# Optimization experiments

Measured on AMD Instinct MI355X. Metric: run time of the kernel, lower is better.

The kernel has to match this reference:

```python
import jax, jax.numpy as jnp
import numpy as np

I_DIM, L_DIM, H_DIM, O_DIM = 1024, 1024, 2048, 512
HALT_H = max(4, H_DIM // 2)
BATCH = 4096


def setup_inputs() -> dict:
    key = jax.random.key(0)
    ks = jax.random.split(key, 14)
    s = 0.02
    gin = I_DIM + O_DIM
    jdim = L_DIM + O_DIM
    return {
        "inputs": jax.random.normal(ks[0], (BATCH, I_DIM), jnp.float32),
        "W_ih": jax.random.normal(ks[1], (3 * L_DIM, gin), jnp.float32) * s,
        "W_hh": jax.random.normal(ks[2], (3 * L_DIM, L_DIM), jnp.float32) * s,
        "b_ih": jax.random.normal(ks[3], (3 * L_DIM,), jnp.float32) * s,
        "b_hh": jax.random.normal(ks[4], (3 * L_DIM,), jnp.float32) * s,
        "aw1": jax.random.normal(ks[5], (H_DIM, jdim), jnp.float32) * s,
        "ab1": jax.random.normal(ks[6], (H_DIM,), jnp.float32) * s,
        "aw2": jax.random.normal(ks[7], (O_DIM, H_DIM), jnp.float32) * s,
        "ab2": jax.random.normal(ks[8], (O_DIM,), jnp.float32) * s,
        "hw1": jax.random.normal(ks[9], (HALT_H, jdim), jnp.float32) * s,
        "hb1": jax.random.normal(ks[10], (HALT_H,), jnp.float32) * s,
        "hw2": jax.random.normal(ks[11], (2, HALT_H), jnp.float32) * s,
        "hb2": jax.random.normal(ks[12], (2,), jnp.float32) * s,
        "inner_cycles": 4,
        "outer_steps": 8,
    }


def reference(inputs, W_ih, W_hh, b_ih, b_hh, aw1, ab1, aw2, ab2,
              hw1, hb1, hw2, hb2, inner_cycles, outer_steps):
    B = inputs.shape[0]
    L = W_hh.shape[1]
    O = aw2.shape[0]

    def gru_step(state, x_gates):
        # PyTorch GRUCell: gates ordered (r, z, n)
        h_gates = state @ W_hh.T + b_hh  # [B, 3L]
        xr, xz, xn = jnp.split(x_gates, 3, axis=-1)
        hr, hz, hn = jnp.split(h_gates, 3, axis=-1)
        r = jax.nn.sigmoid(xr + hr)
        z = jax.nn.sigmoid(xz + hz)
        n = jnp.tanh(xn + r * hn)
        return (1.0 - z) * n + z * state

    def outer(carry, _):
        state, ans = carry
        # gru_input is constant over inner cycles -> hoist input projection
        x = jnp.concatenate([inputs, ans], axis=-1)       # [B, I+O]
        x_gates = x @ W_ih.T + b_ih                        # [B, 3L]

        def inner(s, _):
            return gru_step(s, x_gates), None

        state, _ = jax.lax.scan(inner, state, None, length=inner_cycles)
        joint = jnp.concatenate([state, ans], axis=-1)     # [B, L+O]
        h1 = jax.nn.relu(joint @ aw1.T + ab1)
        logits = h1 @ aw2.T + ab2                          # [B, O]
        ans_new = jnp.tanh(logits)
        h2 = jax.nn.relu(joint @ hw1.T + hb1)
        halt = h2 @ hw2.T + hb2                            # [B, 2]
        return (state, ans_new), (logits, halt)

    state0 = jnp.zeros((B, L), inputs.dtype)
    ans0 = jnp.zeros((B, O), inputs.dtype)
    _, (answer_logits, halt_logits) = jax.lax.scan(
        outer, (state0, ans0), None, length=outer_steps)
    # stacked equivalents of the per-step lists: [outer_steps, B, O], [outer_steps, B, 2]
    return answer_logits, halt_logits
```

## Files before the change

kernel.cpp:

```cpp
#include <hip/hip_runtime.h>
#include <math.h>

#define BATCH 4096
#define LDIM 1024
#define HDIM 2048
#define ODIM 512
#define GDIM 3072
#define JDIM 1536
#define INNER 4
#define OUTER 8

using f16 = _Float16;
using f16x4 = __attribute__((ext_vector_type(4))) _Float16;
using f16x8 = __attribute__((ext_vector_type(8))) _Float16;
using f32x4 = __attribute__((ext_vector_type(4))) float;

typedef __attribute__((address_space(3))) void lds_void;
typedef __attribute__((address_space(1))) void glob_void;

__device__ __forceinline__ void gload16(const void* g, void* l) {
  __builtin_amdgcn_global_load_lds((const glob_void*)g, (lds_void*)l, 16, 0, 0);
}

#define MFMA16(a, b, c) __builtin_amdgcn_mfma_f32_16x16x32_f16(a, b, c, 0, 0, 0)
#define WAIT_VM(N) asm volatile("s_waitcnt vmcnt(" #N ")" ::: "memory")
#define SBAR asm volatile("s_barrier" ::: "memory")

__device__ __forceinline__ float fast_sigmoid(float x) {
  return __builtin_amdgcn_rcpf(1.0f + __expf(-x));
}
__device__ __forceinline__ float fast_tanh(float x) {
  return 1.0f - 2.0f * __builtin_amdgcn_rcpf(1.0f + __expf(2.0f * x));
}

__global__ __launch_bounds__(256) void convert_w(const float* __restrict__ src,
                                                 f16* __restrict__ dst, int n4) {
  int i = blockIdx.x * 256 + threadIdx.x;
  if (i >= n4) return;
  float4 v = ((const float4*)src)[i];
  f16x4 d = {(f16)v.x, (f16)v.y, (f16)v.z, (f16)v.w};
  *(f16x4*)&dst[(size_t)i * 4] = d;
}

__global__ __launch_bounds__(256) void input_to_cat(
    const float* __restrict__ inp, f16* __restrict__ cH) {
  int idx = blockIdx.x * 256 + threadIdx.x;
  if (idx >= BATCH * 256) return;
  int row = idx >> 8, c4 = idx & 255;
  float4 v = ((const float4*)inp)[idx];
  f16x4 h4 = {(f16)v.x, (f16)v.y, (f16)v.z, (f16)v.w};
  *(f16x4*)&cH[(size_t)row * JDIM + c4 * 4] = h4;
}

template <int EPI>
__global__ __launch_bounds__(512, 1) void gemm_f16(
    const f16* __restrict__ A, const f16* __restrict__ W,
    const float* __restrict__ bias, const float* __restrict__ bias2,
    f16* __restrict__ Ch, float* __restrict__ Cf, int N, int K) {
  __shared__ f16 sA[2 * 2 * 256 * 32];
  __shared__ f16 sW[2 * 2 * 256 * 32];
  const int tid = threadIdx.x;
  const int w = tid >> 6, lane = tid & 63;
  const int wm = w >> 2, wn = w & 3;
  const int fr = lane & 15, quad = lane >> 4;
  const int nb = N >> 8;
  const int m0 = (blockIdx.x / nb) * 256, n0 = (blockIdx.x % nb) * 256;

  const int swz_src = (((tid & 3) ^ ((tid >> 3) & 3)) * 8);
  const f16* pAst = A + (size_t)(m0 + (tid >> 2)) * K + swz_src;
  const f16* pWst = W + (size_t)(n0 + (tid >> 2)) * K + swz_src;
  const size_t h128 = (size_t)128 * K;
  const int ldst = tid * 8;
  const int swr = ((quad ^ ((fr >> 1) & 3)) * 8);

  f32x4 acc[8][4] = {};
  const int NT = K >> 6;

#define STA(p, kh, kt)                                              \
  {                                                                 \
    int o = ((p) * 2 + (kh)) * 8192 + ldst;                         \
    gload16(pAst + (kt) * 64 + (kh) * 32, &sA[o]);                  \
    gload16(pAst + h128 + (kt) * 64 + (kh) * 32, &sA[o + 4096]);    \
  }
#define STW(p, kh, kt)                                              \
  {                                                                 \
    int o = ((p) * 2 + (kh)) * 8192 + ldst;                         \
    gload16(pWst + (kt) * 64 + (kh) * 32, &sW[o]);                  \
    gload16(pWst + h128 + (kt) * 64 + (kh) * 32, &sW[o + 4096]);    \
  }
#define LDB(p, kk)                                                  \
  _Pragma("unroll") for (int j = 0; j < 4; ++j) {                   \
    int rn = wn * 64 + j * 16 + fr;                                 \
    bf[j] = *(const f16x8*)&sW[((p) * 2 + (kk)) * 8192 + rn * 32 + swr]; \
  }
#define LDA(p, kk, mh)                                              \
  _Pragma("unroll") for (int i2 = 0; i2 < 4; ++i2) {                \
    int rm = wm * 128 + (mh) * 64 + i2 * 16 + fr;                   \
    af[i2] = *(const f16x8*)&sA[((p) * 2 + (kk)) * 8192 + rm * 32 + swr]; \
  }
#define DOMFMA(mh)                                                  \
  __builtin_amdgcn_s_setprio(1);                                    \
  _Pragma("unroll") for (int i2 = 0; i2 < 4; ++i2)                  \
  _Pragma("unroll") for (int j = 0; j < 4; ++j)                     \
      acc[(mh) * 4 + i2][j] = MFMA16(af[i2], bf[j], acc[(mh) * 4 + i2][j]); \
  __builtin_amdgcn_s_setprio(0);

  STA(0, 0, 0); STW(0, 0, 0); STA(0, 1, 0); STW(0, 1, 0);

  for (int t = 0; t < NT; ++t) {
    const int p = t & 1, pn = p ^ 1;
    const bool pf = (t + 1 < NT);
    f16x8 af[4], bf[4];
    if (t == NT - 1) { WAIT_VM(0); } else { WAIT_VM(4); }
    SBAR;
    if (pf) STA(pn, 0, t + 1);
    LDB(p, 0); LDA(p, 0, 0);
    DOMFMA(0);
    SBAR;
    if (pf) STW(pn, 0, t + 1);
    LDA(p, 0, 1);
    DOMFMA(1);
    if (t == NT - 1) { WAIT_VM(0); } else { WAIT_VM(4); }
    SBAR;
    if (pf) STA(pn, 1, t + 1);
    LDB(p, 1); LDA(p, 1, 0);
    DOMFMA(0);
    SBAR;
    if (pf) STW(pn, 1, t + 1);
    LDA(p, 1, 1);
    DOMFMA(1);
  }
#undef STA
#undef STW
#undef LDB
#undef LDA
#undef DOMFMA

  bool is_h1 = true;
  const float* bp = bias;
  int nb0 = n0;
  if (EPI == 1) {
    is_h1 = (n0 < 2048);
    bp = is_h1 ? bias : bias2;
    nb0 = is_h1 ? n0 : n0 - 2048;
  }
#pragma unroll
  for (int j = 0; j < 4; ++j) {
    int n = nb0 + wn * 64 + j * 16 + fr;
    float bv = bp[n];
#pragma unroll
    for (int i = 0; i < 8; ++i) {
      int mb = m0 + wm * 128 + i * 16 + quad * 4;
      if (EPI == 0) {
        f16x4 o = {(f16)(acc[i][j][0] + bv), (f16)(acc[i][j][1] + bv),
                   (f16)(acc[i][j][2] + bv), (f16)(acc[i][j][3] + bv)};
        *(f16x4*)&Ch[((size_t)(mb >> 2) * N + n) * 4] = o;
      } else {
#pragma unroll
        for (int r = 0; r < 4; ++r) {
          int m = mb + r;
          float v = fmaxf(acc[i][j][r] + bv, 0.0f);
          if (is_h1)
            Ch[(size_t)m * HDIM + n] = (f16)v;
          else
            Cf[(size_t)m * LDIM + n] = v;
        }
      }
    }
  }
}

__global__ __launch_bounds__(256, 2) void gemm_logits(
    const f16* __restrict__ A, const f16* __restrict__ W,
    const float* __restrict__ bias, float* __restrict__ Cout,
    f16* __restrict__ aXH, f16* __restrict__ aJH, int N, int K) {
  __shared__ f16 sA[3][128 * 32];
  __shared__ f16 sW[3][128 * 32];
  const int tid = threadIdx.x;
  const int w = tid >> 6, lane = tid & 63;
  const int wm = w >> 1, wn = w & 1;
  const int fr = lane & 15, quad = lane >> 4;
  const int m0 = blockIdx.y * 128, n0 = blockIdx.x * 128;
  const int srow = w * 32 + (lane >> 2);
  const int scol = (((lane & 3) ^ ((lane >> 3) & 3)) * 8);
  const f16* pA = A + (size_t)(m0 + srow) * K + scol;
  const f16* pW = W + (size_t)(n0 + srow) * K + scol;
  const size_t rstep = (size_t)16 * K;
  const int lo = w * 1024;

  f32x4 acc[4][4] = {};
  const int NT = K >> 5;

  auto stage = [&](int b, int k) {
    gload16(pA + k, &sA[b][lo]);
    gload16(pA + rstep + k, &sA[b][lo + 512]);
    gload16(pW + k, &sW[b][lo]);
    gload16(pW + rstep + k, &sW[b][lo + 512]);
  };
  stage(0, 0);
  stage(1, 32);
  int bb = 0;
  for (int t = 0; t < NT; ++t) {
    if (t == NT - 1) { WAIT_VM(0); } else { WAIT_VM(4); }
    __builtin_amdgcn_s_barrier();
    if (t + 2 < NT) {
      int bn = bb + 2; if (bn >= 3) bn -= 3;
      stage(bn, (t + 2) * 32);
    }
    f16x8 af[4], bf[4];
#pragma unroll
    for (int i = 0; i < 4; ++i) {
      int rr = wm * 64 + i * 16 + fr;
      af[i] = *(const f16x8*)&sA[bb][rr * 32 + ((quad ^ ((rr >> 1) & 3)) << 3)];
    }
#pragma unroll
    for (int j = 0; j < 4; ++j) {
      int rr = wn * 64 + j * 16 + fr;
      bf[j] = *(const f16x8*)&sW[bb][rr * 32 + ((quad ^ ((rr >> 1) & 3)) << 3)];
    }
    __builtin_amdgcn_s_setprio(1);
#pragma unroll
    for (int i = 0; i < 4; ++i)
#pragma unroll
      for (int j = 0; j < 4; ++j) acc[i][j] = MFMA16(af[i], bf[j], acc[i][j]);
    __builtin_amdgcn_s_setprio(0);
    if (++bb == 3) bb = 0;
  }

#pragma unroll
  for (int j = 0; j < 4; ++j) {
    int n = n0 + wn * 64 + j * 16 + fr;
    float bv = bias[n];
#pragma unroll
    for (int i = 0; i < 4; ++i) {
      int mb = m0 + wm * 64 + i * 16 + quad * 4;
#pragma unroll
      for (int r = 0; r < 4; ++r) {
        int m = mb + r;
        float v = acc[i][j][r] + bv;
        Cout[(size_t)m * N + n] = v;
        f16 t = (f16)fast_tanh(v);
        size_t c = (size_t)m * JDIM + 1024 + n;
        aXH[c] = t;
        aJH[c] = t;
      }
    }
  }
}

__global__ __launch_bounds__(256, 2) void gru_fused(
    const f16* __restrict__ inH, const f16* __restrict__ Whh,
    const float* __restrict__ bhh, const f16* __restrict__ xgP,
    f16* __restrict__ outH, f16* __restrict__ catJH) {
  __shared__ f16 sA[3][128 * 32];
  __shared__ f16 sW0[3][64 * 32];
  __shared__ f16 sW1[3][64 * 32];
  __shared__ f16 sW2[3][64 * 32];
  const int tid = threadIdx.x;
  const int w = tid >> 6, lane = tid & 63;
  const int fr = lane & 15, quad = lane >> 4;
  const int flat = blockIdx.x;
  const int xcd = flat & 7, local = flat >> 3;
  const int n0 = (xcd * 2 + (local & 1)) * 64;
  const int m0 = (local >> 1) * 128;
  const int srow = w * 32 + (lane >> 2);
  const int scol = (((lane & 3) ^ ((lane >> 3) & 3)) * 8);
  const f16* pA = inH + (size_t)(m0 + srow) * LDIM + scol;
  const size_t rstepA = (size_t)16 * LDIM;
  const int wrow = w * 16 + (lane >> 2);
  const f16* pW0 = Whh + (size_t)(n0 + wrow) * LDIM + scol;
  const f16* pW1 = pW0 + (size_t)LDIM * LDIM;
  const f16* pW2 = pW1 + (size_t)LDIM * LDIM;
  const int loA = w * 1024, loW = w * 512;

  f32x4 ar[2][4] = {}, az[2][4] = {}, an_[2][4] = {};
  const int NT = LDIM >> 5;

  auto stage = [&](int b, int k) {
    gload16(pA + k, &sA[b][loA]);
    gload16(pA + rstepA + k, &sA[b][loA + 512]);
    gload16(pW0 + k, &sW0[b][loW]);
    gload16(pW1 + k, &sW1[b][loW]);
    gload16(pW2 + k, &sW2[b][loW]);
  };
  stage(0, 0);
  stage(1, 32);
  int bb = 0;
  for (int t = 0; t < NT; ++t) {
    if (t == NT - 1) { WAIT_VM(0); } else { WAIT_VM(5); }
    __builtin_amdgcn_s_barrier();
    if (t + 2 < NT) {
      int bn = bb + 2; if (bn >= 3) bn -= 3;
      stage(bn, (t + 2) * 32);
    }
    f16x8 a_[2], w0[4], w1[4], w2[4];
#pragma unroll
    for (int i = 0; i < 2; ++i) {
      int rr = w * 32 + i * 16 + fr;
      a_[i] = *(const f16x8*)&sA[bb][rr * 32 + ((quad ^ ((rr >> 1) & 3)) << 3)];
    }
#pragma unroll
    for (int j = 0; j < 4; ++j) {
      int rw = j * 16 + fr;
      int wo = rw * 32 + ((quad ^ ((rw >> 1) & 3)) << 3);
      w0[j] = *(const f16x8*)&sW0[bb][wo];
      w1[j] = *(const f16x8*)&sW1[bb][wo];
      w2[j] = *(const f16x8*)&sW2[bb][wo];
    }
    __builtin_amdgcn_s_setprio(1);
#pragma unroll
    for (int i = 0; i < 2; ++i)
#pragma unroll
      for (int j = 0; j < 4; ++j) {
        ar[i][j] = MFMA16(a_[i], w0[j], ar[i][j]);
        az[i][j] = MFMA16(a_[i], w1[j], az[i][j]);
        an_[i][j] = MFMA16(a_[i], w2[j], an_[i][j]);
      }
    __builtin_amdgcn_s_setprio(0);
    if (++bb == 3) bb = 0;
  }

#pragma unroll
  for (int j = 0; j < 4; ++j) {
    int col = n0 + j * 16 + fr;
    float br = bhh[col], bz = bhh[col + LDIM], bn = bhh[col + 2 * LDIM];
#pragma unroll
    for (int i = 0; i < 2; ++i) {
      int mb = m0 + w * 32 + i * 16 + quad * 4;
      size_t xb = ((size_t)(mb >> 2) * GDIM + col) * 4;
      f16x4 x4r = *(const f16x4*)&xgP[xb];
      f16x4 x4z = *(const f16x4*)&xgP[xb + (size_t)LDIM * 4];
      f16x4 x4n = *(const f16x4*)&xgP[xb + (size_t)2 * LDIM * 4];
#pragma unroll
      for (int r = 0; r < 4; ++r) {
        int m = mb + r;
        size_t si = (size_t)m * LDIM + col;
        float sold = (float)inH[si];
        float rg = fast_sigmoid((float)x4r[r] + ar[i][j][r] + br);
        float zg = fast_sigmoid((float)x4z[r] + az[i][j][r] + bz);
        float ng = fast_tanh((float)x4n[r] + rg * (an_[i][j][r] + bn));
        float o = (1.0f - zg) * ng + zg * sold;
        f16 oh = (f16)o;
        outH[si] = oh;
        if (catJH) catJH[(size_t)m * JDIM + col] = oh;
      }
    }
  }
}

__global__ __launch_bounds__(256) void halt_kernel(
    const float* __restrict__ h2, const float* __restrict__ hw2,
    const float* __restrict__ hb2, float* __restrict__ out) {
  int wave = (blockIdx.x * 256 + threadIdx.x) >> 6;
  int lane = threadIdx.x & 63;
  if (wave >= BATCH) return;
  const float* row = h2 + (size_t)wave * LDIM;
  float s0 = 0.0f, s1 = 0.0f;
#pragma unroll
  for (int k = lane; k < LDIM; k += 64) {
    float v = row[k];
    s0 = fmaf(v, hw2[k], s0);
    s1 = fmaf(v, hw2[LDIM + k], s1);
  }
#pragma unroll
  for (int off = 32; off > 0; off >>= 1) {
    s0 += __shfl_xor(s0, off);
    s1 += __shfl_xor(s1, off);
  }
  if (lane == 0) {
    out[(size_t)wave * 2 + 0] = s0 + hb2[0];
    out[(size_t)wave * 2 + 1] = s1 + hb2[1];
  }
}

extern "C" void kernel_launch(void* const* d_in, const int* in_sizes, int n_in,
                              void* d_out, int out_size, void* d_ws, size_t ws_size,
                              hipStream_t stream) {
  const float* inputs = (const float*)d_in[0];
  const float* W_ih = (const float*)d_in[1];
  const float* W_hh = (const float*)d_in[2];
  const float* b_ih = (const float*)d_in[3];
  const float* b_hh = (const float*)d_in[4];
  const float* aw1 = (const float*)d_in[5];
  const float* ab1 = (const float*)d_in[6];
  const float* aw2 = (const float*)d_in[7];
  const float* ab2 = (const float*)d_in[8];
  const float* hw1 = (const float*)d_in[9];
  const float* hb1 = (const float*)d_in[10];
  const float* hw2 = (const float*)d_in[11];
  const float* hb2 = (const float*)d_in[12];

  float* out = (float*)d_out;
  float* logits_out = out;
  float* halt_out = out + (size_t)OUTER * BATCH * ODIM;

  char* p = (char*)d_ws;
  auto take = [&](size_t bytes) { char* q = p; p += (bytes + 255) & ~255ull; return q; };
  f16* stA = (f16*)take((size_t)BATCH * LDIM * 2);
  f16* stB = (f16*)take((size_t)BATCH * LDIM * 2);
  f16* catX = (f16*)take((size_t)BATCH * JDIM * 2);
  f16* catJ = (f16*)take((size_t)BATCH * JDIM * 2);
  f16* xg = (f16*)take((size_t)BATCH * GDIM * 2);
  float* h2F = (float*)take((size_t)BATCH * LDIM * 4);
  f16* WihF = (f16*)take((size_t)GDIM * JDIM * 2);
  f16* WhhF = (f16*)take((size_t)GDIM * LDIM * 2);
  f16* WjF = (f16*)take((size_t)(HDIM + LDIM) * JDIM * 2);
  f16* aw2F = (f16*)take((size_t)ODIM * HDIM * 2);
  f16* h1 = xg;

  (void)hipMemsetAsync(stA, 0, (size_t)BATCH * LDIM * 2, stream);
  (void)hipMemsetAsync(catX, 0, (size_t)BATCH * JDIM * 2, stream);
  (void)hipMemsetAsync(catJ, 0, (size_t)BATCH * JDIM * 2, stream);

  auto conv = [&](const float* s, f16* d, size_t n) {
    int n4 = (int)(n / 4);
    convert_w<<<(n4 + 255) / 256, 256, 0, stream>>>(s, d, n4);
  };
  conv(W_ih, WihF, (size_t)GDIM * JDIM);
  conv(W_hh, WhhF, (size_t)GDIM * LDIM);
  conv(aw1, WjF, (size_t)HDIM * JDIM);
  conv(hw1, WjF + (size_t)HDIM * JDIM, (size_t)LDIM * JDIM);
  conv(aw2, aw2F, (size_t)ODIM * HDIM);
  input_to_cat<<<BATCH, 256, 0, stream>>>(inputs, catX);

  for (int s = 0; s < OUTER; ++s) {
    gemm_f16<0><<<(BATCH / 256) * (GDIM / 256), 512, 0, stream>>>(
        catX, WihF, b_ih, nullptr, xg, nullptr, GDIM, JDIM);
    f16 *cur = stA, *nxt = stB;
    for (int c = 0; c < INNER; ++c) {
      bool last = (c == INNER - 1);
      gru_fused<<<512, 256, 0, stream>>>(
          cur, WhhF, b_hh, xg, nxt, last ? catJ : nullptr);
      f16* t = cur; cur = nxt; nxt = t;
    }
    gemm_f16<1><<<(BATCH / 256) * ((HDIM + LDIM) / 256), 512, 0, stream>>>(
        catJ, WjF, ab1, hb1, h1, h2F, HDIM + LDIM, JDIM);
    gemm_logits<<<dim3(ODIM / 128, BATCH / 128), 256, 0, stream>>>(
        h1, aw2F, ab2, logits_out + (size_t)s * BATCH * ODIM, catX, catJ,
        ODIM, HDIM);
    halt_kernel<<<BATCH / 4, 256, 0, stream>>>(
        h2F, hw2, hb2, halt_out + (size_t)s * BATCH * 2);
  }
}
```

Before: 2.834 ms.

## Split input projection into a hoisted input part and a per-step answer part

The input projection is split so that the fixed inputs@W_ih[:, :1024]+b_ih term is computed once before the outer loop. Each later step then only runs a K=512 GEMM over the answer columns and adds that precomputed base in the epilogue. The GRU state now lives directly inside the joint [state|ans] buffer, so the separate catX/catJ copies and duplicate stores go away, and the halt hidden activations are stored as f16 instead of f32. The trade-offs are an extra full-size xg read in each step's epilogue, the extra rounding from storing h2 in f16, and sharing the xg workspace region with the temporary input and weight conversions.

```diff
diff --git a/kernel.cpp b/kernel.cpp
--- a/kernel.cpp
+++ b/kernel.cpp
@@ -42,21 +42,22 @@
   *(f16x4*)&dst[(size_t)i * 4] = d;
 }
 
-__global__ __launch_bounds__(256) void input_to_cat(
-    const float* __restrict__ inp, f16* __restrict__ cH) {
+__global__ __launch_bounds__(256) void convert_w2(const float* __restrict__ src,
+                                                  f16* __restrict__ dst) {
   int idx = blockIdx.x * 256 + threadIdx.x;
-  if (idx >= BATCH * 256) return;
-  int row = idx >> 8, c4 = idx & 255;
-  float4 v = ((const float4*)inp)[idx];
-  f16x4 h4 = {(f16)v.x, (f16)v.y, (f16)v.z, (f16)v.w};
-  *(f16x4*)&cH[(size_t)row * JDIM + c4 * 4] = h4;
+  if (idx >= GDIM * 128) return;
+  int row = idx >> 7, c4 = idx & 127;
+  float4 v = *(const float4*)&src[(size_t)row * JDIM + 1024 + c4 * 4];
+  f16x4 d = {(f16)v.x, (f16)v.y, (f16)v.z, (f16)v.w};
+  *(f16x4*)&dst[(size_t)row * 512 + c4 * 4] = d;
 }
 
 template <int EPI>
 __global__ __launch_bounds__(512, 1) void gemm_f16(
     const f16* __restrict__ A, const f16* __restrict__ W,
     const float* __restrict__ bias, const float* __restrict__ bias2,
-    f16* __restrict__ Ch, float* __restrict__ Cf, int N, int K) {
+    const f16* __restrict__ Xb,
+    f16* __restrict__ Ch, f16* __restrict__ Cf, int N, int K, int lda, int ldw) {
   __shared__ f16 sA[2 * 2 * 256 * 32];
   __shared__ f16 sW[2 * 2 * 256 * 32];
   const int tid = threadIdx.x;
@@ -67,9 +68,10 @@
   const int m0 = (blockIdx.x / nb) * 256, n0 = (blockIdx.x % nb) * 256;
 
   const int swz_src = (((tid & 3) ^ ((tid >> 3) & 3)) * 8);
-  const f16* pAst = A + (size_t)(m0 + (tid >> 2)) * K + swz_src;
-  const f16* pWst = W + (size_t)(n0 + (tid >> 2)) * K + swz_src;
-  const size_t h128 = (size_t)128 * K;
+  const f16* pAst = A + (size_t)(m0 + (tid >> 2)) * lda + swz_src;
+  const f16* pWst = W + (size_t)(n0 + (tid >> 2)) * ldw + swz_src;
+  const size_t h128a = (size_t)128 * lda;
+  const size_t h128w = (size_t)128 * ldw;
   const int ldst = tid * 8;
   const int swr = ((quad ^ ((fr >> 1) & 3)) * 8);
 
@@ -80,13 +82,13 @@
   {                                                                 \
     int o = ((p) * 2 + (kh)) * 8192 + ldst;                         \
     gload16(pAst + (kt) * 64 + (kh) * 32, &sA[o]);                  \
-    gload16(pAst + h128 + (kt) * 64 + (kh) * 32, &sA[o + 4096]);    \
+    gload16(pAst + h128a + (kt) * 64 + (kh) * 32, &sA[o + 4096]);   \
   }
 #define STW(p, kh, kt)                                              \
   {                                                                 \
     int o = ((p) * 2 + (kh)) * 8192 + ldst;                         \
     gload16(pWst + (kt) * 64 + (kh) * 32, &sW[o]);                  \
-    gload16(pWst + h128 + (kt) * 64 + (kh) * 32, &sW[o + 4096]);    \
+    gload16(pWst + h128w + (kt) * 64 + (kh) * 32, &sW[o + 4096]);   \
   }
 #define LDB(p, kk)                                                  \
   _Pragma("unroll") for (int j = 0; j < 4; ++j) {                   \
@@ -147,7 +149,7 @@
 #pragma unroll
   for (int j = 0; j < 4; ++j) {
     int n = nb0 + wn * 64 + j * 16 + fr;
-    float bv = bp[n];
+    float bv = (EPI == 3) ? 0.0f : bp[n];
 #pragma unroll
     for (int i = 0; i < 8; ++i) {
       int mb = m0 + wm * 128 + i * 16 + quad * 4;
@@ -155,6 +157,14 @@
         f16x4 o = {(f16)(acc[i][j][0] + bv), (f16)(acc[i][j][1] + bv),
                    (f16)(acc[i][j][2] + bv), (f16)(acc[i][j][3] + bv)};
         *(f16x4*)&Ch[((size_t)(mb >> 2) * N + n) * 4] = o;
+      } else if (EPI == 3) {
+        size_t off = ((size_t)(mb >> 2) * N + n) * 4;
+        f16x4 b4 = *(const f16x4*)&Xb[off];
+        f16x4 o = {(f16)(acc[i][j][0] + (float)b4[0]),
+                   (f16)(acc[i][j][1] + (float)b4[1]),
+                   (f16)(acc[i][j][2] + (float)b4[2]),
+                   (f16)(acc[i][j][3] + (float)b4[3])};
+        *(f16x4*)&Ch[off] = o;
       } else {
 #pragma unroll
         for (int r = 0; r < 4; ++r) {
@@ -163,7 +173,7 @@
           if (is_h1)
             Ch[(size_t)m * HDIM + n] = (f16)v;
           else
-            Cf[(size_t)m * LDIM + n] = v;
+            Cf[(size_t)m * LDIM + n] = (f16)v;
         }
       }
     }
@@ -173,7 +183,7 @@
 __global__ __launch_bounds__(256, 2) void gemm_logits(
     const f16* __restrict__ A, const f16* __restrict__ W,
     const float* __restrict__ bias, float* __restrict__ Cout,
-    f16* __restrict__ aXH, f16* __restrict__ aJH, int N, int K) {
+    f16* __restrict__ aJH, int N, int K) {
   __shared__ f16 sA[3][128 * 32];
   __shared__ f16 sW[3][128 * 32];
   const int tid = threadIdx.x;
@@ -239,19 +249,16 @@
         int m = mb + r;
         float v = acc[i][j][r] + bv;
         Cout[(size_t)m * N + n] = v;
-        f16 t = (f16)fast_tanh(v);
-        size_t c = (size_t)m * JDIM + 1024 + n;
-        aXH[c] = t;
-        aJH[c] = t;
+        aJH[(size_t)m * JDIM + 1024 + n] = (f16)fast_tanh(v);
       }
     }
   }
 }
 
 __global__ __launch_bounds__(256, 2) void gru_fused(
-    const f16* __restrict__ inH, const f16* __restrict__ Whh,
+    const f16* __restrict__ inJ, const f16* __restrict__ Whh,
     const float* __restrict__ bhh, const f16* __restrict__ xgP,
-    f16* __restrict__ outH, f16* __restrict__ catJH) {
+    f16* __restrict__ outJ) {
   __shared__ f16 sA[3][128 * 32];
   __shared__ f16 sW0[3][64 * 32];
   __shared__ f16 sW1[3][64 * 32];
@@ -265,8 +272,8 @@
   const int m0 = (local >> 1) * 128;
   const int srow = w * 32 + (lane >> 2);
   const int scol = (((lane & 3) ^ ((lane >> 3) & 3)) * 8);
-  const f16* pA = inH + (size_t)(m0 + srow) * LDIM + scol;
-  const size_t rstepA = (size_t)16 * LDIM;
+  const f16* pA = inJ + (size_t)(m0 + srow) * JDIM + scol;
+  const size_t rstepA = (size_t)16 * JDIM;
   const int wrow = w * 16 + (lane >> 2);
   const f16* pW0 = Whh + (size_t)(n0 + wrow) * LDIM + scol;
   const f16* pW1 = pW0 + (size_t)LDIM * LDIM;
@@ -334,31 +341,29 @@
 #pragma unroll
       for (int r = 0; r < 4; ++r) {
         int m = mb + r;
-        size_t si = (size_t)m * LDIM + col;
-        float sold = (float)inH[si];
+        size_t si = (size_t)m * JDIM + col;
+        float sold = (float)inJ[si];
         float rg = fast_sigmoid((float)x4r[r] + ar[i][j][r] + br);
         float zg = fast_sigmoid((float)x4z[r] + az[i][j][r] + bz);
         float ng = fast_tanh((float)x4n[r] + rg * (an_[i][j][r] + bn));
         float o = (1.0f - zg) * ng + zg * sold;
-        f16 oh = (f16)o;
-        outH[si] = oh;
-        if (catJH) catJH[(size_t)m * JDIM + col] = oh;
+        outJ[si] = (f16)o;
       }
     }
   }
 }
 
 __global__ __launch_bounds__(256) void halt_kernel(
-    const float* __restrict__ h2, const float* __restrict__ hw2,
+    const f16* __restrict__ h2, const float* __restrict__ hw2,
     const float* __restrict__ hb2, float* __restrict__ out) {
   int wave = (blockIdx.x * 256 + threadIdx.x) >> 6;
   int lane = threadIdx.x & 63;
   if (wave >= BATCH) return;
-  const float* row = h2 + (size_t)wave * LDIM;
+  const f16* row = h2 + (size_t)wave * LDIM;
   float s0 = 0.0f, s1 = 0.0f;
 #pragma unroll
   for (int k = lane; k < LDIM; k += 64) {
-    float v = row[k];
+    float v = (float)row[k];
     s0 = fmaf(v, hw2[k], s0);
     s1 = fmaf(v, hw2[LDIM + k], s1);
   }
@@ -396,48 +401,54 @@
 
   char* p = (char*)d_ws;
   auto take = [&](size_t bytes) { char* q = p; p += (bytes + 255) & ~255ull; return q; };
-  f16* stA = (f16*)take((size_t)BATCH * LDIM * 2);
-  f16* stB = (f16*)take((size_t)BATCH * LDIM * 2);
-  f16* catX = (f16*)take((size_t)BATCH * JDIM * 2);
-  f16* catJ = (f16*)take((size_t)BATCH * JDIM * 2);
   f16* xg = (f16*)take((size_t)BATCH * GDIM * 2);
-  float* h2F = (float*)take((size_t)BATCH * LDIM * 4);
-  f16* WihF = (f16*)take((size_t)GDIM * JDIM * 2);
+  f16* inpF16 = xg;
+  f16* WihF = xg + (size_t)BATCH * LDIM;
+  f16* xgBase = (f16*)take((size_t)BATCH * GDIM * 2);
+  f16* J0 = (f16*)take((size_t)BATCH * JDIM * 2);
+  f16* J1 = (f16*)take((size_t)BATCH * JDIM * 2);
+  f16* h2F = (f16*)take((size_t)BATCH * LDIM * 2);
   f16* WhhF = (f16*)take((size_t)GDIM * LDIM * 2);
   f16* WjF = (f16*)take((size_t)(HDIM + LDIM) * JDIM * 2);
   f16* aw2F = (f16*)take((size_t)ODIM * HDIM * 2);
+  f16* W2F = (f16*)take((size_t)GDIM * 512 * 2);
   f16* h1 = xg;
-
-  (void)hipMemsetAsync(stA, 0, (size_t)BATCH * LDIM * 2, stream);
-  (void)hipMemsetAsync(catX, 0, (size_t)BATCH * JDIM * 2, stream);
-  (void)hipMemsetAsync(catJ, 0, (size_t)BATCH * JDIM * 2, stream);
+  if ((size_t)(p - (char*)d_ws) > ws_size) return;
+
+  (void)hipMemsetAsync(J0, 0, (size_t)BATCH * JDIM * 2, stream);
 
   auto conv = [&](const float* s, f16* d, size_t n) {
     int n4 = (int)(n / 4);
     convert_w<<<(n4 + 255) / 256, 256, 0, stream>>>(s, d, n4);
   };
+  conv(inputs, inpF16, (size_t)BATCH * LDIM);
   conv(W_ih, WihF, (size_t)GDIM * JDIM);
+  convert_w2<<<(GDIM * 128 + 255) / 256, 256, 0, stream>>>(W_ih, W2F);
   conv(W_hh, WhhF, (size_t)GDIM * LDIM);
   conv(aw1, WjF, (size_t)HDIM * JDIM);
   conv(hw1, WjF + (size_t)HDIM * JDIM, (size_t)LDIM * JDIM);
   conv(aw2, aw2F, (size_t)ODIM * HDIM);
-  input_to_cat<<<BATCH, 256, 0, stream>>>(inputs, catX);
+
+  gemm_f16<0><<<(BATCH / 256) * (GDIM / 256), 512, 0, stream>>>(
+      inpF16, WihF, b_ih, nullptr, nullptr, xgBase, nullptr,
+      GDIM, LDIM, LDIM, JDIM);
 
   for (int s = 0; s < OUTER; ++s) {
-    gemm_f16<0><<<(BATCH / 256) * (GDIM / 256), 512, 0, stream>>>(
-        catX, WihF, b_ih, nullptr, xg, nullptr, GDIM, JDIM);
-    f16 *cur = stA, *nxt = stB;
-    for (int c = 0; c < INNER; ++c) {
-      bool last = (c == INNER - 1);
-      gru_fused<<<512, 256, 0, stream>>>(
-          cur, WhhF, b_hh, xg, nxt, last ? catJ : nullptr);
-      f16* t = cur; cur = nxt; nxt = t;
-    }
+    const f16* xgUse = xgBase;
+    if (s > 0) {
+      gemm_f16<3><<<(BATCH / 256) * (GDIM / 256), 512, 0, stream>>>(
+          J0 + 1024, W2F, nullptr, nullptr, xgBase, xg, nullptr,
+          GDIM, 512, JDIM, 512);
+      xgUse = xg;
+    }
+    gru_fused<<<512, 256, 0, stream>>>(J0, WhhF, b_hh, xgUse, J1);
+    gru_fused<<<512, 256, 0, stream>>>(J1, WhhF, b_hh, xgUse, J0);
+    gru_fused<<<512, 256, 0, stream>>>(J0, WhhF, b_hh, xgUse, J1);
+    gru_fused<<<512, 256, 0, stream>>>(J1, WhhF, b_hh, xgUse, J0);
     gemm_f16<1><<<(BATCH / 256) * ((HDIM + LDIM) / 256), 512, 0, stream>>>(
-        catJ, WjF, ab1, hb1, h1, h2F, HDIM + LDIM, JDIM);
+        J0, WjF, ab1, hb1, nullptr, h1, h2F, HDIM + LDIM, JDIM, JDIM, JDIM);
     gemm_logits<<<dim3(ODIM / 128, BATCH / 128), 256, 0, stream>>>(
-        h1, aw2F, ab2, logits_out + (size_t)s * BATCH * ODIM, catX, catJ,
-        ODIM, HDIM);
+        h1, aw2F, ab2, logits_out + (size_t)s * BATCH * ODIM, J0, ODIM, HDIM);
     halt_kernel<<<BATCH / 4, 256, 0, stream>>>(
         h2F, hw2, hb2, halt_out + (size_t)s * BATCH * 2);
   }
```

After: 2.532 ms. 10.7% less time.
